# Kernel tuning notes

Measured on AMD Instinct MI355X. Metric: run time of the kernel, lower is better.

## Reference

```python
import jax, jax.numpy as jnp
import numpy as np

N, E, HEADS = 50000, 800000, 4
IN_C, HID_C, OUT_C = 128, 64, 40
WIDTH = HEADS * HID_C  # 256
NEG_SLOPE = 0.2
BN_EPS = 1e-5


def setup_inputs() -> dict:
    key = jax.random.key(0)
    ks = jax.random.split(key, 16)
    s = 0.05
    inp = {
        "x": jax.random.normal(ks[0], (N, IN_C), jnp.float32),
        "edge_index": jax.random.randint(ks[1], (2, E), 0, N, jnp.int32),
        # layer 0: in -> (heads, hid), concat
        "W0": jax.random.normal(ks[2], (IN_C, WIDTH), jnp.float32) * s,
        "a_src0": jax.random.normal(ks[3], (HEADS, HID_C), jnp.float32) * s,
        "a_dst0": jax.random.normal(ks[4], (HEADS, HID_C), jnp.float32) * s,
        "b0": jnp.zeros((WIDTH,), jnp.float32),
        "g0": jnp.ones((WIDTH,), jnp.float32),
        "beta0": jnp.zeros((WIDTH,), jnp.float32),
        # layer 1: width -> (heads, hid), concat
        "W1": jax.random.normal(ks[5], (WIDTH, WIDTH), jnp.float32) * s,
        "a_src1": jax.random.normal(ks[6], (HEADS, HID_C), jnp.float32) * s,
        "a_dst1": jax.random.normal(ks[7], (HEADS, HID_C), jnp.float32) * s,
        "b1": jnp.zeros((WIDTH,), jnp.float32),
        "g1": jnp.ones((WIDTH,), jnp.float32),
        "beta1": jnp.zeros((WIDTH,), jnp.float32),
        # layer 2: width -> (heads, out), mean over heads (concat=False)
        "W2": jax.random.normal(ks[8], (WIDTH, HEADS * OUT_C), jnp.float32) * s,
        "a_src2": jax.random.normal(ks[9], (HEADS, OUT_C), jnp.float32) * s,
        "a_dst2": jax.random.normal(ks[10], (HEADS, OUT_C), jnp.float32) * s,
        "b2": jnp.zeros((OUT_C,), jnp.float32),
    }
    return inp


def _gat_layer(x, W, a_src, a_dst, b, src, dst, out_c, concat):
    # x: [N, F_in]; W: [F_in, HEADS*out_c]
    h = (x @ W).reshape(N, HEADS, out_c)              # [N, H, C]
    e_src = jnp.sum(h * a_src, axis=-1)               # [N, H]
    e_dst = jnp.sum(h * a_dst, axis=-1)               # [N, H]
    e = jax.nn.leaky_relu(e_src[src] + e_dst[dst], NEG_SLOPE)  # [E', H]
    # segment softmax over incoming edges of each destination node
    m = jax.ops.segment_max(e, dst, num_segments=N)
    e = jnp.exp(e - m[dst])
    z = jax.ops.segment_sum(e, dst, num_segments=N)
    alpha = e / (z[dst] + 1e-16)                      # [E', H]
    msg = h[src] * alpha[:, :, None]                  # [E', H, C]
    out = jax.ops.segment_sum(msg, dst, num_segments=N)  # [N, H, C]
    if concat:
        return out.reshape(N, HEADS * out_c) + b
    return out.mean(axis=1) + b


def _batchnorm(x, g, beta):
    mu = x.mean(axis=0)
    var = x.var(axis=0)
    return (x - mu) * jax.lax.rsqrt(var + BN_EPS) * g + beta


def reference(x, edge_index, W0, a_src0, a_dst0, b0, g0, beta0,
              W1, a_src1, a_dst1, b1, g1, beta1,
              W2, a_src2, a_dst2, b2):
    # add self-loops (PyG GATConv default)
    loops = jnp.arange(N, dtype=edge_index.dtype)
    src = jnp.concatenate([edge_index[0], loops])
    dst = jnp.concatenate([edge_index[1], loops])

    h = _gat_layer(x, W0, a_src0, a_dst0, b0, src, dst, HID_C, True)
    h = jax.nn.elu(_batchnorm(h, g0, beta0))
    h = _gat_layer(h, W1, a_src1, a_dst1, b1, src, dst, HID_C, True)
    h = jax.nn.elu(_batchnorm(h, g1, beta1))
    h = _gat_layer(h, W2, a_src2, a_dst2, b2, src, dst, OUT_C, False)
    return jax.nn.log_softmax(h, axis=-1)
```

## Files before the change

kernel.cpp:

```cpp
#include <hip/hip_runtime.h>

#define NN 50000
#define EE 800000
#define NEP (EE + NN)
#define NBS 512

typedef float f32x4 __attribute__((ext_vector_type(4)));
typedef short bf16x8 __attribute__((ext_vector_type(8)));

__device__ inline float bf2f(unsigned short u) {
    union { unsigned int i; float f; } v; v.i = ((unsigned int)u) << 16; return v.f;
}
__device__ inline float lo2f(unsigned int u) {
    return __builtin_bit_cast(float, u << 16);
}
__device__ inline float hi2f(unsigned int u) {
    return __builtin_bit_cast(float, u & 0xFFFF0000u);
}
__device__ inline unsigned short f2bf(float f) {
    unsigned int x = __builtin_bit_cast(unsigned int, f);
    unsigned int r = x + 0x7FFFu + ((x >> 16) & 1u);
    return (unsigned short)(r >> 16);
}

__global__ __launch_bounds__(256) void k_cs(const int* __restrict__ ei,
                                            int* __restrict__ counts, int* __restrict__ lps) {
    int e = blockIdx.x * 256 + threadIdx.x;
    if (e >= NEP) return;
    int dst = (e < EE) ? ei[EE + e] : (e - EE);
    lps[e] = atomicAdd(&counts[dst], 1);
}

__global__ __launch_bounds__(1024) void k_scan(const int* __restrict__ counts,
                                               int* __restrict__ indptr) {
    __shared__ int wsum[16];
    __shared__ int carry_s;
    int tid = threadIdx.x, lane = tid & 63, wid = tid >> 6;
    if (tid == 0) carry_s = 0;
    __syncthreads();
    for (int base = 0; base < NN; base += 1024) {
        int i = base + tid;
        int v = (i < NN) ? counts[i] : 0;
        int s = v;
        #pragma unroll
        for (int d = 1; d < 64; d <<= 1) { int t = __shfl_up(s, d); if (lane >= d) s += t; }
        if (lane == 63) wsum[wid] = s;
        __syncthreads();
        if (wid == 0) {
            int ws = (lane < 16) ? wsum[lane] : 0;
            #pragma unroll
            for (int d = 1; d < 16; d <<= 1) { int t = __shfl_up(ws, d); if (lane >= d) ws += t; }
            if (lane < 16) wsum[lane] = ws;
        }
        __syncthreads();
        int off = carry_s + (wid > 0 ? wsum[wid - 1] : 0);
        int excl = off + s - v;
        if (i < NN) indptr[i] = excl;
        __syncthreads();
        if (tid == 1023) carry_s = off + s;
        __syncthreads();
    }
    if (tid == 0) indptr[NN] = carry_s;
}

__global__ __launch_bounds__(256) void k_place(const int* __restrict__ ei,
                                               const int* __restrict__ indptr,
                                               const int* __restrict__ lps,
                                               int* __restrict__ srcs) {
    int e = blockIdx.x * 256 + threadIdx.x;
    if (e >= NEP) return;
    int src, dst;
    if (e < EE) { src = ei[e]; dst = ei[EE + e]; }
    else        { src = e - EE; dst = src; }
    srcs[indptr[dst] + lps[e]] = src;
}

__global__ __launch_bounds__(256) void k_expand(const int* __restrict__ indptr,
                                                int* __restrict__ dstc) {
    const int wid = threadIdx.x >> 6, lane = threadIdx.x & 63;
    const int n = blockIdx.x * 4 + wid;
    if (n >= NN) return;
    const int e0 = __builtin_amdgcn_readfirstlane(indptr[n]);
    const int e1 = __builtin_amdgcn_readfirstlane(indptr[n + 1]);
    for (int e = e0 + lane; e < e1; e += 64) dstc[e] = n;
}

#define XN4 1600000
__global__ __launch_bounds__(256) void k_prep(const float* __restrict__ x, unsigned short* __restrict__ xb,
        const float* __restrict__ W0, unsigned short* __restrict__ Wt0,
        const float* __restrict__ W1, unsigned short* __restrict__ Wt1,
        const float* __restrict__ W2, unsigned short* __restrict__ Wt2,
        const float* __restrict__ vs0, const float* __restrict__ vd0,
        float4* __restrict__ es4, float4* __restrict__ ed4) {
    int i = blockIdx.x * 256 + threadIdx.x;
    if (i < XN4) {
        float4 v = ((const float4*)x)[i];
        ushort4 o;
        o.x = f2bf(v.x); o.y = f2bf(v.y); o.z = f2bf(v.z); o.w = f2bf(v.w);
        ((ushort4*)xb)[i] = o;
        const int k0 = (i & 31) * 4;
        const float vv[4] = {v.x, v.y, v.z, v.w};
        float s[4] = {0.f, 0.f, 0.f, 0.f}, dd[4] = {0.f, 0.f, 0.f, 0.f};
        #pragma unroll
        for (int j = 0; j < 4; j++) {
            float f = vv[j];
            float4 a = *(const float4*)&vs0[(k0 + j) * 4];
            float4 b = *(const float4*)&vd0[(k0 + j) * 4];
            s[0] += f * a.x; s[1] += f * a.y; s[2] += f * a.z; s[3] += f * a.w;
            dd[0] += f * b.x; dd[1] += f * b.y; dd[2] += f * b.z; dd[3] += f * b.w;
        }
        #pragma unroll
        for (int d = 1; d < 32; d <<= 1) {
            #pragma unroll
            for (int j = 0; j < 4; j++) { s[j] += __shfl_xor(s[j], d); dd[j] += __shfl_xor(dd[j], d); }
        }
        if ((threadIdx.x & 31) == 0) {
            int row = i >> 5;
            es4[row] = make_float4(s[0], s[1], s[2], s[3]);
            ed4[row] = make_float4(dd[0], dd[1], dd[2], dd[3]);
        }
        return;
    }
    i -= XN4;
    if (i < 256 * 128) {
        int c = i >> 7, k = i & 127;
        Wt0[i] = f2bf(W0[(size_t)k * 256 + c]);
        return;
    }
    i -= 256 * 128;
    if (i < 256 * 256) {
        int c = i >> 8, k = i & 255;
        Wt1[i] = f2bf(W1[(size_t)k * 256 + c]);
        return;
    }
    i -= 256 * 256;
    if (i < 192 * 256) {
        int c = i >> 8, k = i & 255;
        Wt2[i] = f2bf((c < 160) ? W2[(size_t)k * 160 + c] : 0.f);
    }
}

__global__ __launch_bounds__(256) void k_wv(
        const float* __restrict__ W0, const float* __restrict__ as0, const float* __restrict__ ad0,
        const float* __restrict__ W1, const float* __restrict__ as1, const float* __restrict__ ad1,
        const float* __restrict__ W2, const float* __restrict__ as2, const float* __restrict__ ad2,
        float* __restrict__ vs0, float* __restrict__ vd0,
        float* __restrict__ vs1, float* __restrict__ vd1,
        float* __restrict__ vs2, float* __restrict__ vd2) {
    int b = blockIdx.x;
    const float *W, *as_, *ad_; float *vs, *vd; int k, C, NO;
    if (b < 128)      { W = W0; as_ = as0; ad_ = ad0; vs = vs0; vd = vd0; k = b;       C = 64; NO = 256; }
    else if (b < 384) { W = W1; as_ = as1; ad_ = ad1; vs = vs1; vd = vd1; k = b - 128; C = 64; NO = 256; }
    else              { W = W2; as_ = as2; ad_ = ad2; vs = vs2; vd = vd2; k = b - 384; C = 40; NO = 160; }
    int h = threadIdx.x >> 6, c = threadIdx.x & 63;
    float s1 = 0.f, s2 = 0.f;
    if (c < C) {
        float wv = W[(size_t)k * NO + h * C + c];
        s1 = wv * as_[h * C + c];
        s2 = wv * ad_[h * C + c];
    }
    #pragma unroll
    for (int d = 1; d < 64; d <<= 1) { s1 += __shfl_xor(s1, d); s2 += __shfl_xor(s2, d); }
    if (c == 0) { vs[k * 4 + h] = s1; vd[k * 4 + h] = s2; }
}

__global__ __launch_bounds__(256) void k_wgt(const float4* __restrict__ es4,
        const float4* __restrict__ ed4, const int* __restrict__ srcs,
        const int* __restrict__ dstc, uint2* __restrict__ wq) {
    int p = blockIdx.x * 256 + threadIdx.x;
    if (p >= NEP) return;
    float4 s = es4[srcs[p]];
    float4 d = ed4[dstc[p]];
    float e0 = s.x + d.x, e1 = s.y + d.y, e2 = s.z + d.z, e3 = s.w + d.w;
    e0 = (e0 > 0.f) ? e0 : 0.2f * e0;
    e1 = (e1 > 0.f) ? e1 : 0.2f * e1;
    e2 = (e2 > 0.f) ? e2 : 0.2f * e2;
    e3 = (e3 > 0.f) ? e3 : 0.2f * e3;
    uint2 o;
    o.x = (unsigned int)f2bf(__expf(e0)) | ((unsigned int)f2bf(__expf(e1)) << 16);
    o.y = (unsigned int)f2bf(__expf(e2)) | ((unsigned int)f2bf(__expf(e3)) << 16);
    wq[p] = o;
}

template<int K, int NOUTP, int NO>
__global__ __launch_bounds__(256) void k_gemm(const unsigned short* __restrict__ Xb,
                                              const unsigned short* __restrict__ Wt,
                                              unsigned char* __restrict__ Y) {
    constexpr int G = K / 8;
    __shared__ __attribute__((aligned(16))) unsigned short As[64 * K];
    const int bm = blockIdx.x * 64;
    const int tid = threadIdx.x, lane = tid & 63, wid = tid >> 6;
    const int wm = wid >> 1, wn = wid & 1;
    const int l15 = lane & 15, l4 = lane >> 4;

    #pragma unroll
    for (int i = 0; i < (64 * G) / 256; i++) {
        int p = tid + 256 * i;
        int row = p / G, g = p % G;
        int grow = bm + row; if (grow >= NN) grow = 0;
        int gsrc = g ^ (row & 7);
        const unsigned short* gp = &Xb[(size_t)grow * K + gsrc * 8];
        __builtin_amdgcn_global_load_lds(
            (const __attribute__((address_space(1))) void*)gp,
            (__attribute__((address_space(3))) void*)&As[p * 8],
            16, 0, 0);
    }
    __syncthreads();

    #pragma unroll
    for (int bg = 0; bg < NOUTP / 64; bg++) {
        const int bn = bg * 64;
        bf16x8 bfr[2][K / 32];
        #pragma unroll
        for (int n = 0; n < 2; n++) {
            const int col = bn + wn * 32 + n * 16 + l15;
            #pragma unroll
            for (int ks = 0; ks < K / 32; ks++)
                bfr[n][ks] = *(const bf16x8*)&Wt[(size_t)col * K + ks * 32 + l4 * 8];
        }
        f32x4 acc[2][2];
        #pragma unroll
        for (int m = 0; m < 2; m++)
            #pragma unroll
            for (int n = 0; n < 2; n++) acc[m][n] = (f32x4)0.f;
        #pragma unroll
        for (int ks = 0; ks < K / 32; ks++) {
            #pragma unroll
            for (int m = 0; m < 2; m++) {
                const int r = wm * 32 + m * 16 + l15;
                const int pg = ((ks << 2) + l4) ^ (r & 7);
                bf16x8 af = *(const bf16x8*)&As[r * K + pg * 8];
                #pragma unroll
                for (int n = 0; n < 2; n++)
                    acc[m][n] = __builtin_amdgcn_mfma_f32_16x16x32_bf16(af, bfr[n][ks], acc[m][n], 0, 0, 0);
            }
        }
        #pragma unroll
        for (int m = 0; m < 2; m++) {
            const int row0 = bm + wm * 32 + m * 16 + l4 * 4;
            #pragma unroll
            for (int n = 0; n < 2; n++) {
                const int col = bn + wn * 32 + n * 16 + l15;
                if (col >= NO) continue;
                #pragma unroll
                for (int j = 0; j < 4; j++) {
                    int gr = row0 + j;
                    if (gr >= NN) continue;
                    int pk = __builtin_amdgcn_cvt_pk_fp8_f32(acc[m][n][j], acc[m][n][j], 0, false);
                    Y[(size_t)gr * NOUTP + col] = (unsigned char)pk;
                }
            }
        }
    }
}

__global__ __launch_bounds__(256) void k_agg(const unsigned char* __restrict__ H,
        const uint2* __restrict__ wq,
        const int* __restrict__ indptr, const int* __restrict__ srcs,
        unsigned short* __restrict__ outp) {
    const int wid = threadIdx.x >> 6, lane = threadIdx.x & 63;
    const int n = blockIdx.x * 4 + wid;
    if (n >= NN) return;
    const int head = lane >> 4;
    const int hw = head >> 1, hs = (head & 1) * 16;
    const int e0 = __builtin_amdgcn_readfirstlane(indptr[n]);
    const int e1 = __builtin_amdgcn_readfirstlane(indptr[n + 1]);
    float z = 0.f, a0 = 0.f, a1 = 0.f, a2 = 0.f, a3 = 0.f;
    const unsigned char* Hp = H + lane * 4;
    int e = e0;
    for (; e + 8 <= e1; e += 8) {
        int s[8]; float ww[8];
        #pragma unroll
        for (int q = 0; q < 8; q++) {
            s[q] = srcs[e + q];
            uint2 w2 = wq[e + q];
            unsigned int ws = hw ? w2.y : w2.x;
            ww[q] = bf2f((unsigned short)(ws >> hs));
        }
        #pragma unroll
        for (int q = 0; q < 8; q++) {
            unsigned int hv = *(const unsigned int*)(Hp + (size_t)s[q] * 256);
            z += ww[q];
            a0 += ww[q] * __builtin_amdgcn_cvt_f32_fp8(hv, 0);
            a1 += ww[q] * __builtin_amdgcn_cvt_f32_fp8(hv, 1);
            a2 += ww[q] * __builtin_amdgcn_cvt_f32_fp8(hv, 2);
            a3 += ww[q] * __builtin_amdgcn_cvt_f32_fp8(hv, 3);
        }
    }
    for (; e < e1; ++e) {
        int s0 = srcs[e];
        uint2 w2 = wq[e];
        unsigned int ws = hw ? w2.y : w2.x;
        float w0 = bf2f((unsigned short)(ws >> hs));
        unsigned int hv = *(const unsigned int*)(Hp + (size_t)s0 * 256);
        z += w0;
        a0 += w0 * __builtin_amdgcn_cvt_f32_fp8(hv, 0);
        a1 += w0 * __builtin_amdgcn_cvt_f32_fp8(hv, 1);
        a2 += w0 * __builtin_amdgcn_cvt_f32_fp8(hv, 2);
        a3 += w0 * __builtin_amdgcn_cvt_f32_fp8(hv, 3);
    }
    float inv = 1.f / (z + 1e-16f);
    ushort4 o;
    o.x = f2bf(a0 * inv); o.y = f2bf(a1 * inv); o.z = f2bf(a2 * inv); o.w = f2bf(a3 * inv);
    *(ushort4*)&outp[(size_t)n * 256 + lane * 4] = o;
}

__global__ __launch_bounds__(256) void k_agg2(const unsigned char* __restrict__ H2,
        const uint2* __restrict__ wq,
        const int* __restrict__ indptr, const int* __restrict__ srcs,
        const float* __restrict__ b2, float* __restrict__ outp) {
    const int wid = threadIdx.x >> 6, lane = threadIdx.x & 63;
    const int n = blockIdx.x * 4 + wid;
    if (n >= NN) return;
    const bool act = lane < 40;
    const int head = lane / 10;
    const int hw = head >> 1, hs = (head & 1) * 16;
    const int e0 = __builtin_amdgcn_readfirstlane(indptr[n]);
    const int e1 = __builtin_amdgcn_readfirstlane(indptr[n + 1]);
    float z = 0.f, acc[4] = {0.f, 0.f, 0.f, 0.f};
    const unsigned char* Hp = H2 + lane * 4;
    if (act) {
        int e = e0;
        for (; e + 8 <= e1; e += 8) {
            int s[8]; float ww[8];
            #pragma unroll
            for (int q = 0; q < 8; q++) {
                s[q] = srcs[e + q];
                uint2 w2 = wq[e + q];
                unsigned int ws = hw ? w2.y : w2.x;
                ww[q] = bf2f((unsigned short)(ws >> hs));
            }
            #pragma unroll
            for (int q = 0; q < 8; q++) {
                unsigned int hv = *(const unsigned int*)(Hp + (size_t)s[q] * 192);
                z += ww[q];
                acc[0] += ww[q] * __builtin_amdgcn_cvt_f32_fp8(hv, 0);
                acc[1] += ww[q] * __builtin_amdgcn_cvt_f32_fp8(hv, 1);
                acc[2] += ww[q] * __builtin_amdgcn_cvt_f32_fp8(hv, 2);
                acc[3] += ww[q] * __builtin_amdgcn_cvt_f32_fp8(hv, 3);
            }
        }
        for (; e < e1; ++e) {
            int s0 = srcs[e];
            uint2 w2 = wq[e];
            unsigned int ws = hw ? w2.y : w2.x;
            float w0 = bf2f((unsigned short)(ws >> hs));
            unsigned int hv = *(const unsigned int*)(Hp + (size_t)s0 * 192);
            z += w0;
            acc[0] += w0 * __builtin_amdgcn_cvt_f32_fp8(hv, 0);
            acc[1] += w0 * __builtin_amdgcn_cvt_f32_fp8(hv, 1);
            acc[2] += w0 * __builtin_amdgcn_cvt_f32_fp8(hv, 2);
            acc[3] += w0 * __builtin_amdgcn_cvt_f32_fp8(hv, 3);
        }
    }
    float inv = 1.f / (z + 1e-16f);
    float sv[4];
    #pragma unroll
    for (int j = 0; j < 4; j++) sv[j] = acc[j] * inv;
    #pragma unroll
    for (int j = 0; j < 4; j++) {
        float v = sv[j];
        v += __shfl(sv[j], lane + 10);
        v += __shfl(sv[j], lane + 20);
        v += __shfl(sv[j], lane + 30);
        sv[j] = v;
    }
    const bool ol = lane < 10;
    float m4 = -1e30f;
    #pragma unroll
    for (int j = 0; j < 4; j++) {
        sv[j] = ol ? (0.25f * sv[j] + b2[lane * 4 + j]) : -1e30f;
        m4 = fmaxf(m4, sv[j]);
    }
    #pragma unroll
    for (int d = 1; d < 16; d <<= 1) m4 = fmaxf(m4, __shfl_xor(m4, d));
    float s = 0.f;
    #pragma unroll
    for (int j = 0; j < 4; j++) s += ol ? __expf(sv[j] - m4) : 0.f;
    #pragma unroll
    for (int d = 1; d < 16; d <<= 1) s += __shfl_xor(s, d);
    float ls = logf(s);
    if (ol) {
        float4 o = make_float4(sv[0] - m4 - ls, sv[1] - m4 - ls, sv[2] - m4 - ls, sv[3] - m4 - ls);
        *(float4*)&outp[(size_t)n * 40 + lane * 4] = o;
    }
}

__global__ __launch_bounds__(256) void k_bnstats1(const unsigned short* __restrict__ X,
        float* __restrict__ ps, float* __restrict__ pq) {
    __shared__ float lds[4 * 256];
    const int tid = threadIdx.x;
    const int colg = (tid & 63) * 4;
    const int w = tid >> 6;
    float s[4] = {0.f, 0.f, 0.f, 0.f}, q[4] = {0.f, 0.f, 0.f, 0.f};
    for (int r = blockIdx.x * 4 + w; r < NN; r += NBS * 4) {
        ushort4 hv = *(const ushort4*)&X[(size_t)r * 256 + colg];
        const unsigned short hh[4] = {hv.x, hv.y, hv.z, hv.w};
        #pragma unroll
        for (int j = 0; j < 4; j++) { float v = bf2f(hh[j]); s[j] += v; q[j] += v * v; }
    }
    #pragma unroll
    for (int j = 0; j < 4; j++) lds[w * 256 + colg + j] = s[j];
    __syncthreads();
    float ts = lds[tid] + lds[256 + tid] + lds[512 + tid] + lds[768 + tid];
    __syncthreads();
    #pragma unroll
    for (int j = 0; j < 4; j++) lds[w * 256 + colg + j] = q[j];
    __syncthreads();
    float tq = lds[tid] + lds[256 + tid] + lds[512 + tid] + lds[768 + tid];
    ps[(size_t)blockIdx.x * 256 + tid] = ts;
    pq[(size_t)blockIdx.x * 256 + tid] = tq;
}

__global__ __launch_bounds__(256) void k_bnred(const float* __restrict__ ps,
        const float* __restrict__ pq, const float* __restrict__ g,
        const float* __restrict__ beta, float* __restrict__ sc_o, float* __restrict__ sh_o) {
    const int col = blockIdx.x, tid = threadIdx.x;
    float s = ps[(size_t)tid * 256 + col] + ps[(size_t)(tid + 256) * 256 + col];
    float q = pq[(size_t)tid * 256 + col] + pq[(size_t)(tid + 256) * 256 + col];
    #pragma unroll
    for (int d = 1; d < 64; d <<= 1) { s += __shfl_xor(s, d); q += __shfl_xor(q, d); }
    __shared__ float ls[4], lq[4];
    if ((tid & 63) == 0) { ls[tid >> 6] = s; lq[tid >> 6] = q; }
    __syncthreads();
    if (tid == 0) {
        float S = ls[0] + ls[1] + ls[2] + ls[3];
        float Q = lq[0] + lq[1] + lq[2] + lq[3];
        const float inv = 1.f / (float)NN;
        float mu = S * inv;
        float var = Q * inv - mu * mu;
        float sc = rsqrtf(var + 1e-5f) * g[col];
        sc_o[col] = sc;
        sh_o[col] = beta[col] - mu * sc;
    }
}

__global__ __launch_bounds__(256) void k_bnapply(unsigned short* __restrict__ X,
        const float* __restrict__ sc_i, const float* __restrict__ sh_i,
        const float* __restrict__ vs, const float* __restrict__ vd,
        float4* __restrict__ es4, float4* __restrict__ ed4) {
    const int hl = threadIdx.x & 31;
    const int colg = hl * 8;
    const int rowo = threadIdx.x >> 5;
    float sc[8], sh[8];
    #pragma unroll
    for (int j = 0; j < 8; j++) { sc[j] = sc_i[colg + j]; sh[j] = sh_i[colg + j]; }
    for (int r = blockIdx.x * 8 + rowo; r < NN; r += gridDim.x * 8) {
        uint4 u = *(uint4*)&X[(size_t)r * 256 + colg];
        unsigned int uu[4] = {u.x, u.y, u.z, u.w};
        unsigned int oo[4];
        float s[4] = {0.f, 0.f, 0.f, 0.f}, dd[4] = {0.f, 0.f, 0.f, 0.f};
        #pragma unroll
        for (int p = 0; p < 4; p++) {
            float lo = lo2f(uu[p]);
            float hi = hi2f(uu[p]);
            float vlo = lo * sc[p * 2] + sh[p * 2];
            float vhi = hi * sc[p * 2 + 1] + sh[p * 2 + 1];
            vlo = (vlo > 0.f) ? vlo : expm1f(vlo);
            vhi = (vhi > 0.f) ? vhi : expm1f(vhi);
            oo[p] = (unsigned int)f2bf(vlo) | ((unsigned int)f2bf(vhi) << 16);
            float4 a0 = *(const float4*)&vs[(colg + 2 * p) * 4];
            float4 b0 = *(const float4*)&vd[(colg + 2 * p) * 4];
            float4 a1 = *(const float4*)&vs[(colg + 2 * p + 1) * 4];
            float4 b1 = *(const float4*)&vd[(colg + 2 * p + 1) * 4];
            s[0] += vlo * a0.x + vhi * a1.x; s[1] += vlo * a0.y + vhi * a1.y;
            s[2] += vlo * a0.z + vhi * a1.z; s[3] += vlo * a0.w + vhi * a1.w;
            dd[0] += vlo * b0.x + vhi * b1.x; dd[1] += vlo * b0.y + vhi * b1.y;
            dd[2] += vlo * b0.z + vhi * b1.z; dd[3] += vlo * b0.w + vhi * b1.w;
        }
        *(uint4*)&X[(size_t)r * 256 + colg] = make_uint4(oo[0], oo[1], oo[2], oo[3]);
        #pragma unroll
        for (int d = 1; d < 32; d <<= 1) {
            #pragma unroll
            for (int j = 0; j < 4; j++) { s[j] += __shfl_xor(s[j], d); dd[j] += __shfl_xor(dd[j], d); }
        }
        if (hl == 0) {
            es4[r] = make_float4(s[0], s[1], s[2], s[3]);
            ed4[r] = make_float4(dd[0], dd[1], dd[2], dd[3]);
        }
    }
}

extern "C" void kernel_launch(void* const* d_in, const int* in_sizes, int n_in,
                              void* d_out, int out_size, void* d_ws, size_t ws_size,
                              hipStream_t stream) {
    const float* x   = (const float*)d_in[0];
    const int*   ei  = (const int*)d_in[1];
    const float* W0  = (const float*)d_in[2];
    const float* as0 = (const float*)d_in[3];
    const float* ad0 = (const float*)d_in[4];
    const float* g0  = (const float*)d_in[6];
    const float* be0 = (const float*)d_in[7];
    const float* W1  = (const float*)d_in[8];
    const float* as1 = (const float*)d_in[9];
    const float* ad1 = (const float*)d_in[10];
    const float* g1  = (const float*)d_in[12];
    const float* be1 = (const float*)d_in[13];
    const float* W2  = (const float*)d_in[14];
    const float* as2 = (const float*)d_in[15];
    const float* ad2 = (const float*)d_in[16];
    const float* b2  = (const float*)d_in[17];
    float* out = (float*)d_out;

    char* w = (char*)d_ws;
    size_t off = 0;
    auto take = [&](size_t bytes) -> void* {
        off = (off + 255) & ~(size_t)255;
        void* p = w + off; off += bytes; return p;
    };
    unsigned short* Agg16 = (unsigned short*)take((size_t)NN * 256 * 2);
    unsigned short* xb    = (unsigned short*)take((size_t)NN * 128 * 2);
    unsigned char*  H8    = (unsigned char*)take((size_t)NN * 256);
    float* es     = (float*)take((size_t)NN * 4 * 4);
    float* ed     = (float*)take((size_t)NN * 4 * 4);
    int*   counts = (int*)take((size_t)NN * 4);
    int*   indptr = (int*)take((size_t)(NN + 1) * 4);
    int*   lps    = (int*)take((size_t)NEP * 4);
    int*   srcs   = (int*)take((size_t)NEP * 4);
    int*   dstc   = (int*)take((size_t)NEP * 4);
    uint2* wq     = (uint2*)take((size_t)NEP * 8);
    unsigned short* Wt0 = (unsigned short*)take((size_t)256 * 128 * 2);
    unsigned short* Wt1 = (unsigned short*)take((size_t)256 * 256 * 2);
    unsigned short* Wt2 = (unsigned short*)take((size_t)192 * 256 * 2);
    float* vs0 = (float*)take(128 * 4 * 4);
    float* vd0 = (float*)take(128 * 4 * 4);
    float* vs1 = (float*)take(256 * 4 * 4);
    float* vd1 = (float*)take(256 * 4 * 4);
    float* vs2 = (float*)take(256 * 4 * 4);
    float* vd2 = (float*)take(256 * 4 * 4);
    float* ps  = (float*)take((size_t)NBS * 256 * 4);
    float* pq  = (float*)take((size_t)NBS * 256 * 4);
    float* bns = (float*)take(512 * 4);

    const int gE = (NEP + 255) / 256;
    const int gPrep = (XN4 + 256 * 128 + 256 * 256 + 192 * 256 + 255) / 256;

    k_wv<<<640, 256, 0, stream>>>(W0, as0, ad0, W1, as1, ad1, W2, as2, ad2,
                                  vs0, vd0, vs1, vd1, vs2, vd2);
    k_prep<<<gPrep, 256, 0, stream>>>(x, xb, W0, Wt0, W1, Wt1, W2, Wt2,
                                      vs0, vd0, (float4*)es, (float4*)ed);

    hipMemsetAsync(counts, 0, (size_t)NN * 4, stream);
    k_cs    <<<gE, 256, 0, stream>>>(ei, counts, lps);
    k_scan  <<<1, 1024, 0, stream>>>(counts, indptr);
    k_place <<<gE, 256, 0, stream>>>(ei, indptr, lps, srcs);

    const int gM = (NN + 63) / 64;
    const int gW = (NN + 3) / 4;

    k_expand<<<gW, 256, 0, stream>>>(indptr, dstc);

    k_wgt<<<gE, 256, 0, stream>>>((const float4*)es, (const float4*)ed, srcs, dstc, wq);
    k_gemm<128, 256, 256><<<gM, 256, 0, stream>>>(xb, Wt0, H8);
    k_agg<<<gW, 256, 0, stream>>>(H8, wq, indptr, srcs, Agg16);
    k_bnstats1<<<NBS, 256, 0, stream>>>(Agg16, ps, pq);
    k_bnred<<<256, 256, 0, stream>>>(ps, pq, g0, be0, bns, bns + 256);
    k_bnapply<<<1024, 256, 0, stream>>>(Agg16, bns, bns + 256, vs1, vd1,
                                        (float4*)es, (float4*)ed);

    k_wgt<<<gE, 256, 0, stream>>>((const float4*)es, (const float4*)ed, srcs, dstc, wq);
    k_gemm<256, 256, 256><<<gM, 256, 0, stream>>>(Agg16, Wt1, H8);
    k_agg<<<gW, 256, 0, stream>>>(H8, wq, indptr, srcs, Agg16);
    k_bnstats1<<<NBS, 256, 0, stream>>>(Agg16, ps, pq);
    k_bnred<<<256, 256, 0, stream>>>(ps, pq, g1, be1, bns, bns + 256);
    k_bnapply<<<1024, 256, 0, stream>>>(Agg16, bns, bns + 256, vs2, vd2,
                                        (float4*)es, (float4*)ed);

    k_wgt<<<gE, 256, 0, stream>>>((const float4*)es, (const float4*)ed, srcs, dstc, wq);
    k_gemm<256, 192, 160><<<gM, 256, 0, stream>>>(Agg16, Wt2, H8);
    k_agg2<<<gW, 256, 0, stream>>>(H8, wq, indptr, srcs, b2, out);
}
```

Measured before the change: 420.6 us.

## Replace single-block serial scan with three-pass multi-block prefix scan

The exclusive prefix sum over per-node edge counts ran in one 1024-thread block that looped about 49 times with several barriers per iteration. It is now split into three kernels: per-block local scans with int4 loads, a one-wave scan of the block totals, and a pass that adds each block's offset. This spreads the scan across many CUs and removes the serial loop, at the cost of two extra kernel launches.

```diff
diff --git a/kernel.cpp b/kernel.cpp
--- a/kernel.cpp
+++ b/kernel.cpp
@@ -4,6 +4,7 @@
 #define EE 800000
 #define NEP (EE + NN)
 #define NBS 512
+#define SCB 49
 
 typedef float f32x4 __attribute__((ext_vector_type(4)));
 typedef short bf16x8 __attribute__((ext_vector_type(8)));
@@ -31,36 +32,66 @@
     lps[e] = atomicAdd(&counts[dst], 1);
 }
 
-__global__ __launch_bounds__(1024) void k_scan(const int* __restrict__ counts,
-                                               int* __restrict__ indptr) {
-    __shared__ int wsum[16];
-    __shared__ int carry_s;
-    int tid = threadIdx.x, lane = tid & 63, wid = tid >> 6;
-    if (tid == 0) carry_s = 0;
+__global__ __launch_bounds__(256) void k_scan1(const int* __restrict__ counts,
+                                               int* __restrict__ indptr, int* __restrict__ bsum) {
+    const int tid = threadIdx.x, lane = tid & 63, wid = tid >> 6;
+    const int base = blockIdx.x * 1024 + tid * 4;
+    int4 v = make_int4(0, 0, 0, 0);
+    if (base + 3 < NN) v = *(const int4*)&counts[base];
+    else {
+        if (base + 0 < NN) v.x = counts[base + 0];
+        if (base + 1 < NN) v.y = counts[base + 1];
+        if (base + 2 < NN) v.z = counts[base + 2];
+        if (base + 3 < NN) v.w = counts[base + 3];
+    }
+    int t = v.x + v.y + v.z + v.w;
+    int s = t;
+    #pragma unroll
+    for (int d = 1; d < 64; d <<= 1) { int u = __shfl_up(s, d); if (lane >= d) s += u; }
+    __shared__ int ws[4], wo[4];
+    if (lane == 63) ws[wid] = s;
     __syncthreads();
-    for (int base = 0; base < NN; base += 1024) {
-        int i = base + tid;
-        int v = (i < NN) ? counts[i] : 0;
-        int s = v;
-        #pragma unroll
-        for (int d = 1; d < 64; d <<= 1) { int t = __shfl_up(s, d); if (lane >= d) s += t; }
-        if (lane == 63) wsum[wid] = s;
-        __syncthreads();
-        if (wid == 0) {
-            int ws = (lane < 16) ? wsum[lane] : 0;
-            #pragma unroll
-            for (int d = 1; d < 16; d <<= 1) { int t = __shfl_up(ws, d); if (lane >= d) ws += t; }
-            if (lane < 16) wsum[lane] = ws;
-        }
-        __syncthreads();
-        int off = carry_s + (wid > 0 ? wsum[wid - 1] : 0);
-        int excl = off + s - v;
-        if (i < NN) indptr[i] = excl;
-        __syncthreads();
-        if (tid == 1023) carry_s = off + s;
-        __syncthreads();
-    }
-    if (tid == 0) indptr[NN] = carry_s;
+    if (tid == 0) {
+        int a = 0;
+        #pragma unroll
+        for (int j = 0; j < 4; j++) { wo[j] = a; a += ws[j]; }
+        bsum[blockIdx.x] = a;
+    }
+    __syncthreads();
+    int excl = wo[wid] + s - t;
+    int p0 = excl, p1 = p0 + v.x, p2 = p1 + v.y, p3 = p2 + v.z;
+    if (base + 3 < NN) *(int4*)&indptr[base] = make_int4(p0, p1, p2, p3);
+    else {
+        if (base + 0 < NN) indptr[base + 0] = p0;
+        if (base + 1 < NN) indptr[base + 1] = p1;
+        if (base + 2 < NN) indptr[base + 2] = p2;
+        if (base + 3 < NN) indptr[base + 3] = p3;
+    }
+}
+
+__global__ __launch_bounds__(64) void k_scan2(int* __restrict__ bsum, int* __restrict__ indptr) {
+    const int lane = threadIdx.x;
+    int v = (lane < SCB) ? bsum[lane] : 0;
+    int s = v;
+    #pragma unroll
+    for (int d = 1; d < 64; d <<= 1) { int u = __shfl_up(s, d); if (lane >= d) s += u; }
+    if (lane < SCB) bsum[lane] = s - v;
+    if (lane == SCB - 1) indptr[NN] = s;
+}
+
+__global__ __launch_bounds__(256) void k_scan3(int* __restrict__ indptr, const int* __restrict__ bsum) {
+    const int base = blockIdx.x * 1024 + threadIdx.x * 4;
+    const int off = bsum[blockIdx.x];
+    if (off == 0) return;
+    if (base + 3 < NN) {
+        int4 v = *(const int4*)&indptr[base];
+        v.x += off; v.y += off; v.z += off; v.w += off;
+        *(int4*)&indptr[base] = v;
+    } else {
+        #pragma unroll
+        for (int j = 0; j < 4; j++)
+            if (base + j < NN) indptr[base + j] += off;
+    }
 }
 
 __global__ __launch_bounds__(256) void k_place(const int* __restrict__ ei,
@@ -519,6 +550,7 @@
     int*   srcs   = (int*)take((size_t)NEP * 4);
     int*   dstc   = (int*)take((size_t)NEP * 4);
     uint2* wq     = (uint2*)take((size_t)NEP * 8);
+    int*   bsum   = (int*)take(64 * 4);
     unsigned short* Wt0 = (unsigned short*)take((size_t)256 * 128 * 2);
     unsigned short* Wt1 = (unsigned short*)take((size_t)256 * 256 * 2);
     unsigned short* Wt2 = (unsigned short*)take((size_t)192 * 256 * 2);
@@ -541,9 +573,11 @@
                                       vs0, vd0, (float4*)es, (float4*)ed);
 
     hipMemsetAsync(counts, 0, (size_t)NN * 4, stream);
-    k_cs    <<<gE, 256, 0, stream>>>(ei, counts, lps);
-    k_scan  <<<1, 1024, 0, stream>>>(counts, indptr);
-    k_place <<<gE, 256, 0, stream>>>(ei, indptr, lps, srcs);
+    k_cs   <<<gE, 256, 0, stream>>>(ei, counts, lps);
+    k_scan1<<<SCB, 256, 0, stream>>>(counts, indptr, bsum);
+    k_scan2<<<1, 64, 0, stream>>>(bsum, indptr);
+    k_scan3<<<SCB, 256, 0, stream>>>(indptr, bsum);
+    k_place<<<gE, 256, 0, stream>>>(ei, indptr, lps, srcs);
 
     const int gM = (NN + 63) / 64;
     const int gW = (NN + 3) / 4;
```

After: 380.4 us. 1.11x faster.
